# Optimization experiments

Measured on AMD Instinct MI355X. Metric: run time of the kernel, lower is better.

## Reference

```python
import jax, jax.numpy as jnp
import numpy as np

B, L, V, D = 4096, 128, 50257, 64
NEG_INF = -1e9
COS_EPS = 1e-8  # torch cosine_similarity default eps


def setup_inputs() -> dict:
    key = jax.random.key(0)
    k1, k2, k3, k4, k5, k6 = jax.random.split(key, 6)
    return {
        "ids_a": jax.random.randint(k1, (B, L), 0, V, dtype=jnp.int64) if jax.config.jax_enable_x64 else jax.random.randint(k1, (B, L), 0, V, dtype=jnp.int32),
        "mask_a": jax.random.randint(k2, (B, L), 0, 2, dtype=jnp.int32),
        "ids_b": jax.random.randint(k3, (B, L), 0, V, dtype=jnp.int32),
        "mask_b": jax.random.randint(k4, (B, L), 0, 2, dtype=jnp.int32),
        "mu_table": jax.random.normal(k5, (V, D), dtype=jnp.float32),
        "feat_table": jax.random.normal(k6, (V, D), dtype=jnp.float32),
    }


def _side(ids, mask, mu_table, feat_table):
    # Embedding gathers: [B, L, D]
    mu = mu_table[ids]
    feat = feat_table[ids]
    m = mask.astype(mu.dtype)  # [B, L]
    # render_mean_pool: masked mean of mu -> query [B, D]
    denom = jnp.maximum(m.sum(axis=1, keepdims=True), 1.0)
    q = jnp.einsum('bld,bl->bd', mu, m) / denom
    # render_softmax_attention: single-query masked softmax over mu keys
    scores = jnp.einsum('bld,bd->bl', mu, q)
    scores = jnp.where(mask.astype(bool), scores, NEG_INF)
    attn = jax.nn.softmax(scores, axis=-1)  # [B, L]
    return jnp.einsum('bl,bld->bd', attn, feat)  # weighted sum of feat


def reference(ids_a, mask_a, ids_b, mask_b, mu_table, feat_table):
    mean_a = _side(ids_a, mask_a, mu_table, feat_table)
    mean_b = _side(ids_b, mask_b, mu_table, feat_table)
    # torch cosine_similarity: x.y / (max(||x||, eps) * max(||y||, eps))
    na = jnp.maximum(jnp.linalg.norm(mean_a, axis=-1), COS_EPS)
    nb = jnp.maximum(jnp.linalg.norm(mean_b, axis=-1), COS_EPS)
    cos = jnp.sum(mean_a * mean_b, axis=-1) / (na * nb)
    return cos * 5.0
```

## Files before the change

### kernel.cpp

```cpp
#include <hip/hip_runtime.h>
#include <hip/hip_fp16.h>
#include <math.h>

#define BB 4096
#define LL 128
#define DD 64
#define VV 50257
#define TAB_ELEMS (VV * DD)

typedef _Float16 h2_t __attribute__((ext_vector_type(2)));

__device__ __forceinline__ float dot2acc(unsigned a, unsigned b, float c) {
#if __has_builtin(__builtin_amdgcn_fdot2)
    return __builtin_amdgcn_fdot2(__builtin_bit_cast(h2_t, a),
                                  __builtin_bit_cast(h2_t, b), c, false);
#else
    const float2 fa = __half22float2(*(const __half2*)&a);
    const float2 fb = __half22float2(*(const __half2*)&b);
    return fmaf(fa.x, fb.x, fmaf(fa.y, fb.y, c));
#endif
}

__device__ __forceinline__ float2 cvt2(unsigned raw) {
    return __half22float2(*(const __half2*)&raw);
}

__device__ __forceinline__ unsigned pack_h2(float a, float b) {
    union { __half2 h; unsigned u; } p;
    p.h = __floats2half2_rn(a, b);
    return p.u;
}

__global__ __launch_bounds__(256) void convert_tables_kernel(
    const float* __restrict__ mu, const float* __restrict__ feat,
    __half* __restrict__ out_mu, __half* __restrict__ out_feat)
{
    const int n4 = TAB_ELEMS / 4;
    for (int i = blockIdx.x * blockDim.x + threadIdx.x; i < n4;
         i += gridDim.x * blockDim.x) {
        const float4 m = ((const float4*)mu)[i];
        const float4 f = ((const float4*)feat)[i];
        uint2 pm, pf;
        pm.x = pack_h2(m.x, m.y); pm.y = pack_h2(m.z, m.w);
        pf.x = pack_h2(f.x, f.y); pf.y = pack_h2(f.z, f.w);
        ((uint2*)out_mu)[i]   = pm;
        ((uint2*)out_feat)[i] = pf;
    }
}

__global__ __launch_bounds__(256, 6) void softmax_attn_cos_kernel(
    const int* __restrict__ ids_a, const int* __restrict__ mask_a,
    const int* __restrict__ ids_b, const int* __restrict__ mask_b,
    const __half* __restrict__ mu_table, const __half* __restrict__ feat_table,
    float* __restrict__ out)
{
    __shared__ int      s_cid[2][LL];
    __shared__ int      s_cnt[2][2];
    __shared__ unsigned s_qh[2][32];
    __shared__ float4   s_qp[2][2][16];
    __shared__ float    s_sc[2][LL];
    __shared__ float4   s_op[2][2][16];
    __shared__ float    s_mean[2][DD];
    __shared__ float    s_sum[2];

    const int tid  = threadIdx.x;
    const int lane = tid & 63;
    const int wave = tid >> 6;
    const int side = wave >> 1;
    const int wsub = wave & 1;
    const int r8   = lane >> 3;
    const int c8   = lane & 7;
    const int b    = blockIdx.x;

    {
        const int l = wsub * 64 + lane;
        const int* idp = side ? ids_b  : ids_a;
        const int* mp  = side ? mask_b : mask_a;
        const int id = idp[b * LL + l];
        const int m  = mp[b * LL + l];
        const unsigned long long bal = __ballot(m != 0);
        if (lane == 0) s_cnt[side][wsub] = __popcll(bal);
        const int rank = __popcll(bal & ((1ull << lane) - 1ull));
        __syncthreads();
        const int offset = wsub ? s_cnt[side][0] : 0;
        if (m) s_cid[side][offset + rank] = id;
        if (s_cnt[side][0] + s_cnt[side][1] == 0)
            s_cid[side][l] = id;
    }
    __syncthreads();

    const int   nm  = s_cnt[side][0] + s_cnt[side][1];
    const int   nme = (nm == 0) ? 128 : nm;
    const int   G   = (nme + 7) >> 3;

    uint4 v[8];
    unsigned voff[8];
    {
        float4 qa = make_float4(0.f, 0.f, 0.f, 0.f);
        float4 qb = make_float4(0.f, 0.f, 0.f, 0.f);
        #pragma unroll
        for (int it = 0; it < 8; ++it) {
            v[it] = make_uint4(0u, 0u, 0u, 0u);
            voff[it] = 0u;
            const int g = 2 * it + wsub;
            if (g < G) {
                const int p = g * 8 + r8;
                const int id = (p < nme) ? s_cid[side][p] : 0;
                voff[it] = ((unsigned)id << 7) + ((unsigned)c8 << 4);
                v[it] = *(const uint4*)((const char*)mu_table + voff[it]);
                if (p < nm) {
                    const float2 f0 = cvt2(v[it].x), f1 = cvt2(v[it].y);
                    const float2 f2 = cvt2(v[it].z), f3 = cvt2(v[it].w);
                    qa.x += f0.x; qa.y += f0.y; qa.z += f1.x; qa.w += f1.y;
                    qb.x += f2.x; qb.y += f2.y; qb.z += f3.x; qb.w += f3.y;
                }
            }
        }
        #pragma unroll
        for (int off = 8; off <= 32; off <<= 1) {
            qa.x += __shfl_xor(qa.x, off, 64); qa.y += __shfl_xor(qa.y, off, 64);
            qa.z += __shfl_xor(qa.z, off, 64); qa.w += __shfl_xor(qa.w, off, 64);
            qb.x += __shfl_xor(qb.x, off, 64); qb.y += __shfl_xor(qb.y, off, 64);
            qb.z += __shfl_xor(qb.z, off, 64); qb.w += __shfl_xor(qb.w, off, 64);
        }
        if (lane < 8) {
            s_qp[side][wsub][2 * c8]     = qa;
            s_qp[side][wsub][2 * c8 + 1] = qb;
        }
    }
    __syncthreads();

    if (tid < 128) {
        const int si = tid >> 6;
        const int dd = tid & 63;
        if (dd < 16) {
            const float dn = fmaxf((float)(s_cnt[si][0] + s_cnt[si][1]), 1.0f);
            const float rd = 1.0f / dn;
            const float4 q0 = s_qp[si][0][dd], q1 = s_qp[si][1][dd];
            s_qh[si][2 * dd]     = pack_h2((q0.x + q1.x) * rd, (q0.y + q1.y) * rd);
            s_qh[si][2 * dd + 1] = pack_h2((q0.z + q1.z) * rd, (q0.w + q1.w) * rd);
        }
    }
    __syncthreads();

    {
        const uint4 qq = ((const uint4*)&s_qh[side][0])[c8];
        #pragma unroll
        for (int it = 0; it < 8; ++it) {
            const int g = 2 * it + wsub;
            if (g < G) {
                const int p = g * 8 + r8;
                float sp = dot2acc(v[it].x, qq.x, 0.f);
                sp = dot2acc(v[it].y, qq.y, sp);
                sp = dot2acc(v[it].z, qq.z, sp);
                sp = dot2acc(v[it].w, qq.w, sp);
                const uint4 nf = *(const uint4*)((const char*)feat_table + voff[it]);
                #pragma unroll
                for (int off = 1; off <= 4; off <<= 1)
                    sp += __shfl_xor(sp, off, 64);
                if (c8 == 0 && p < nme) s_sc[side][p] = sp;
                v[it] = nf;
            }
        }
    }
    __syncthreads();

    if (wsub == 0) {
        const float s1 = (lane      < nme) ? s_sc[side][lane]      : -1e9f;
        const float s2 = (lane + 64 < nme) ? s_sc[side][lane + 64] : -1e9f;
        float mx = fmaxf(s1, s2);
        #pragma unroll
        for (int off = 32; off; off >>= 1) mx = fmaxf(mx, __shfl_xor(mx, off, 64));
        const float e1 = expf(s1 - mx), e2 = expf(s2 - mx);
        s_sc[side][lane] = e1; s_sc[side][lane + 64] = e2;
        float sm = e1 + e2;
        #pragma unroll
        for (int off = 32; off; off >>= 1) sm += __shfl_xor(sm, off, 64);
        if (lane == 0) s_sum[side] = sm;
    }
    __syncthreads();

    {
        float4 oa = make_float4(0.f, 0.f, 0.f, 0.f);
        float4 ob = make_float4(0.f, 0.f, 0.f, 0.f);
        #pragma unroll
        for (int it = 0; it < 8; ++it) {
            const int g = 2 * it + wsub;
            if (g < G) {
                const int p = g * 8 + r8;
                const float w = (p < nme) ? s_sc[side][p] : 0.f;
                const float2 f0 = cvt2(v[it].x), f1 = cvt2(v[it].y);
                const float2 f2 = cvt2(v[it].z), f3 = cvt2(v[it].w);
                oa.x = fmaf(f0.x, w, oa.x); oa.y = fmaf(f0.y, w, oa.y);
                oa.z = fmaf(f1.x, w, oa.z); oa.w = fmaf(f1.y, w, oa.w);
                ob.x = fmaf(f2.x, w, ob.x); ob.y = fmaf(f2.y, w, ob.y);
                ob.z = fmaf(f3.x, w, ob.z); ob.w = fmaf(f3.y, w, ob.w);
            }
        }
        #pragma unroll
        for (int off = 8; off <= 32; off <<= 1) {
            oa.x += __shfl_xor(oa.x, off, 64); oa.y += __shfl_xor(oa.y, off, 64);
            oa.z += __shfl_xor(oa.z, off, 64); oa.w += __shfl_xor(oa.w, off, 64);
            ob.x += __shfl_xor(ob.x, off, 64); ob.y += __shfl_xor(ob.y, off, 64);
            ob.z += __shfl_xor(ob.z, off, 64); ob.w += __shfl_xor(ob.w, off, 64);
        }
        if (lane < 8) {
            s_op[side][wsub][2 * c8]     = oa;
            s_op[side][wsub][2 * c8 + 1] = ob;
        }
    }
    __syncthreads();

    if (tid < 32) {
        const int si = tid >> 4, cc = tid & 15;
        const float inv = 1.0f / s_sum[si];
        const float4 o0 = s_op[si][0][cc], o1 = s_op[si][1][cc];
        float4 o;
        o.x = (o0.x + o1.x) * inv; o.y = (o0.y + o1.y) * inv;
        o.z = (o0.z + o1.z) * inv; o.w = (o0.w + o1.w) * inv;
        ((float4*)&s_mean[si][0])[cc] = o;
    }
    __syncthreads();

    if (tid < 64) {
        const float a = s_mean[0][tid], c = s_mean[1][tid];
        float dt = a * c, na = a * a, nb = c * c;
        #pragma unroll
        for (int off = 32; off; off >>= 1) {
            dt += __shfl_xor(dt, off, 64);
            na += __shfl_xor(na, off, 64);
            nb += __shfl_xor(nb, off, 64);
        }
        if (tid == 0) {
            const float denom = fmaxf(sqrtf(na), 1e-8f) * fmaxf(sqrtf(nb), 1e-8f);
            out[b] = 5.0f * dt / denom;
        }
    }
}

extern "C" void kernel_launch(void* const* d_in, const int* in_sizes, int n_in,
                              void* d_out, int out_size, void* d_ws, size_t ws_size,
                              hipStream_t stream) {
    const int*   ids_a  = (const int*)d_in[0];
    const int*   mask_a = (const int*)d_in[1];
    const int*   ids_b  = (const int*)d_in[2];
    const int*   mask_b = (const int*)d_in[3];
    const float* mu     = (const float*)d_in[4];
    const float* feat   = (const float*)d_in[5];
    float* out = (float*)d_out;

    __half* ws_mu   = (__half*)d_ws;
    __half* ws_feat = ws_mu + TAB_ELEMS;

    convert_tables_kernel<<<2048, 256, 0, stream>>>(mu, feat, ws_mu, ws_feat);
    softmax_attn_cos_kernel<<<BB, 256, 0, stream>>>(
        ids_a, mask_a, ids_b, mask_b, ws_mu, ws_feat, out);
}
```

Measured before the change: 110.5 us.

## Interleave mu and feat half tables per row and prefetch both upfront

The conversion kernel now writes one interleaved fp16 table where each vocabulary row holds 128 bytes of mu followed by 128 bytes of feat. The attention kernel loads both halves of a gathered row at the start, so the feat gather comes from the same 256-byte region and overlaps with the mu gather instead of waiting until the score phase. This doubles register use for the prefetched data, which is why launch bounds drop from 6 to 4 blocks per CU and occupancy falls.

```diff
diff --git a/kernel.cpp b/kernel.cpp
--- a/kernel.cpp
+++ b/kernel.cpp
@@ -31,28 +31,30 @@
     return p.u;
 }
 
-__global__ __launch_bounds__(256) void convert_tables_kernel(
+__global__ __launch_bounds__(256) void convert_fused_kernel(
     const float* __restrict__ mu, const float* __restrict__ feat,
-    __half* __restrict__ out_mu, __half* __restrict__ out_feat)
+    __half* __restrict__ out)
 {
-    const int n4 = TAB_ELEMS / 4;
-    for (int i = blockIdx.x * blockDim.x + threadIdx.x; i < n4;
+    const int total = VV * 16;
+    for (int i = blockIdx.x * blockDim.x + threadIdx.x; i < total;
          i += gridDim.x * blockDim.x) {
-        const float4 m = ((const float4*)mu)[i];
-        const float4 f = ((const float4*)feat)[i];
-        uint2 pm, pf;
-        pm.x = pack_h2(m.x, m.y); pm.y = pack_h2(m.z, m.w);
-        pf.x = pack_h2(f.x, f.y); pf.y = pack_h2(f.z, f.w);
-        ((uint2*)out_mu)[i]   = pm;
-        ((uint2*)out_feat)[i] = pf;
-    }
-}
-
-__global__ __launch_bounds__(256, 6) void softmax_attn_cos_kernel(
+        const int row = i >> 4;
+        const int c   = i & 15;
+        const float* src = (c < 8) ? (mu   + row * DD + c * 8)
+                                   : (feat + row * DD + (c - 8) * 8);
+        const float4 s0 = ((const float4*)src)[0];
+        const float4 s1 = ((const float4*)src)[1];
+        uint4 o;
+        o.x = pack_h2(s0.x, s0.y); o.y = pack_h2(s0.z, s0.w);
+        o.z = pack_h2(s1.x, s1.y); o.w = pack_h2(s1.z, s1.w);
+        ((uint4*)out)[i] = o;
+    }
+}
+
+__global__ __launch_bounds__(256, 4) void softmax_attn_cos_kernel(
     const int* __restrict__ ids_a, const int* __restrict__ mask_a,
     const int* __restrict__ ids_b, const int* __restrict__ mask_b,
-    const __half* __restrict__ mu_table, const __half* __restrict__ feat_table,
-    float* __restrict__ out)
+    const __half* __restrict__ fused_table, float* __restrict__ out)
 {
     __shared__ int      s_cid[2][LL];
     __shared__ int      s_cnt[2][2];
@@ -94,26 +96,33 @@
     const int   G   = (nme + 7) >> 3;
 
     uint4 v[8];
-    unsigned voff[8];
-    {
+    uint4 f[8];
+    {
+        #pragma unroll
+        for (int it = 0; it < 8; ++it) {
+            v[it] = make_uint4(0u, 0u, 0u, 0u);
+            f[it] = make_uint4(0u, 0u, 0u, 0u);
+            const int g = 2 * it + wsub;
+            if (g < G) {
+                const int p  = g * 8 + r8;
+                const int id = (p < nme) ? s_cid[side][p] : 0;
+                const char* base = (const char*)fused_table
+                                 + ((unsigned)id << 8) + ((unsigned)c8 << 4);
+                v[it] = *(const uint4*)(base);
+                f[it] = *(const uint4*)(base + 128);
+            }
+        }
         float4 qa = make_float4(0.f, 0.f, 0.f, 0.f);
         float4 qb = make_float4(0.f, 0.f, 0.f, 0.f);
         #pragma unroll
         for (int it = 0; it < 8; ++it) {
-            v[it] = make_uint4(0u, 0u, 0u, 0u);
-            voff[it] = 0u;
-            const int g = 2 * it + wsub;
-            if (g < G) {
-                const int p = g * 8 + r8;
-                const int id = (p < nme) ? s_cid[side][p] : 0;
-                voff[it] = ((unsigned)id << 7) + ((unsigned)c8 << 4);
-                v[it] = *(const uint4*)((const char*)mu_table + voff[it]);
-                if (p < nm) {
-                    const float2 f0 = cvt2(v[it].x), f1 = cvt2(v[it].y);
-                    const float2 f2 = cvt2(v[it].z), f3 = cvt2(v[it].w);
-                    qa.x += f0.x; qa.y += f0.y; qa.z += f1.x; qa.w += f1.y;
-                    qb.x += f2.x; qb.y += f2.y; qb.z += f3.x; qb.w += f3.y;
-                }
+            const int g = 2 * it + wsub;
+            const int p = g * 8 + r8;
+            if (g < G && p < nm) {
+                const float2 f0 = cvt2(v[it].x), f1 = cvt2(v[it].y);
+                const float2 f2 = cvt2(v[it].z), f3 = cvt2(v[it].w);
+                qa.x += f0.x; qa.y += f0.y; qa.z += f1.x; qa.w += f1.y;
+                qb.x += f2.x; qb.y += f2.y; qb.z += f3.x; qb.w += f3.y;
             }
         }
         #pragma unroll
@@ -154,12 +163,10 @@
                 sp = dot2acc(v[it].y, qq.y, sp);
                 sp = dot2acc(v[it].z, qq.z, sp);
                 sp = dot2acc(v[it].w, qq.w, sp);
-                const uint4 nf = *(const uint4*)((const char*)feat_table + voff[it]);
                 #pragma unroll
                 for (int off = 1; off <= 4; off <<= 1)
                     sp += __shfl_xor(sp, off, 64);
                 if (c8 == 0 && p < nme) s_sc[side][p] = sp;
-                v[it] = nf;
             }
         }
     }
@@ -189,8 +196,8 @@
             if (g < G) {
                 const int p = g * 8 + r8;
                 const float w = (p < nme) ? s_sc[side][p] : 0.f;
-                const float2 f0 = cvt2(v[it].x), f1 = cvt2(v[it].y);
-                const float2 f2 = cvt2(v[it].z), f3 = cvt2(v[it].w);
+                const float2 f0 = cvt2(f[it].x), f1 = cvt2(f[it].y);
+                const float2 f2 = cvt2(f[it].z), f3 = cvt2(f[it].w);
                 oa.x = fmaf(f0.x, w, oa.x); oa.y = fmaf(f0.y, w, oa.y);
                 oa.z = fmaf(f1.x, w, oa.z); oa.w = fmaf(f1.y, w, oa.w);
                 ob.x = fmaf(f2.x, w, ob.x); ob.y = fmaf(f2.y, w, ob.y);
@@ -249,10 +256,9 @@
     const float* feat   = (const float*)d_in[5];
     float* out = (float*)d_out;
 
-    __half* ws_mu   = (__half*)d_ws;
-    __half* ws_feat = ws_mu + TAB_ELEMS;
-
-    convert_tables_kernel<<<2048, 256, 0, stream>>>(mu, feat, ws_mu, ws_feat);
+    __half* ws_fused = (__half*)d_ws;
+
+    convert_fused_kernel<<<2048, 256, 0, stream>>>(mu, feat, ws_fused);
     softmax_attn_cos_kernel<<<BB, 256, 0, stream>>>(
-        ids_a, mask_a, ids_b, mask_b, ws_mu, ws_feat, out);
-}
+        ids_a, mask_a, ids_b, mask_b, ws_fused, out);
+}
```

After: 112.5 us. About the same (+1.9%).
